# Kernel tuning notes

Measured on AMD Instinct MI355X. Metric: run time of the kernel, lower is better.

The kernel has to match this reference:

```python
import jax, jax.numpy as jnp
import numpy as np

N = 50000
E = 1600000
IN_F = 512
OUT_F = 128
NEG_SLOPE = 0.01   # nn.LeakyReLU() default
TEMPERATURE = 0.5


def setup_inputs() -> dict:
    key = jax.random.key(0)
    k1, k2, k3, k4 = jax.random.split(key, 4)
    h = jax.random.normal(k1, (N, IN_F), dtype=jnp.float32)
    # xavier_uniform with gain=1.414
    limW = 1.414 * np.sqrt(6.0 / (IN_F + OUT_F))
    W = jax.random.uniform(k2, (IN_F, OUT_F), minval=-limW, maxval=limW, dtype=jnp.float32)
    lima = 1.414 * np.sqrt(6.0 / (2 * OUT_F + 1))
    a = jax.random.uniform(k3, (2 * OUT_F, 1), minval=-lima, maxval=lima, dtype=jnp.float32)
    edge_index = jax.random.randint(k4, (2, E), 0, N, dtype=jnp.int64)
    return {"h": h, "W": W, "a": a, "edge_index": edge_index}


def reference(h, W, a, edge_index):
    # Inference: F.dropout(training=False) is identity.
    Wh = h @ W                                   # [N, F_out]
    src = edge_index[0]                          # row indices -> softmax segments
    dst = edge_index[1]
    # cat([Wh[src], Wh[dst]]) @ a == (Wh @ a1)[src] + (Wh @ a2)[dst]
    a1 = a[:OUT_F, 0]
    a2 = a[OUT_F:, 0]
    s1 = Wh @ a1                                 # [N]
    s2 = Wh @ a2                                 # [N]
    e = s1[src] + s2[dst]                        # [E]
    e = jnp.where(e >= 0, e, NEG_SLOPE * e)      # LeakyReLU
    logits = e / TEMPERATURE
    # sparse softmax over dim=1 (per source-node row segments)
    seg_max = jax.ops.segment_max(logits, src, num_segments=N)  # [N]
    ex = jnp.exp(logits - seg_max[src])          # [E]
    denom = jax.ops.segment_sum(ex, src, num_segments=N)        # [N]
    att = ex / denom[src]                        # [E]
    # sparse-dense matmul: h_prime[i] = sum_j att(i,j) * Wh[j]
    h_prime = jax.ops.segment_sum(att[:, None] * Wh[dst], src, num_segments=N)  # [N, F_out]
    return jax.nn.relu(h_prime)                  # concat=True path
```

## Files before the change

### kernel.cpp

```cpp
#include <hip/hip_runtime.h>
#include <cstdint>
#include <cstddef>

#define N_NODES 50000
#define N_EDGES 1600000
#define IN_FEAT 512
#define OUT_FEAT 128
#define NEG_SLOPE 0.01f
#define INV_TEMP 2.0f
#define PAD_DEG 128

#define BUCKETS 400
#define BNODES 125
#define BCAP 5000
#define A_BLOCKS 250
#define A_EPC (N_EDGES / A_BLOCKS)
#define A_G4 (A_EPC / 4)

typedef __attribute__((ext_vector_type(8))) short short8;
typedef __attribute__((ext_vector_type(4))) float f32x4;

#define GLOBAL_AS __attribute__((address_space(1)))
#define LDS_AS __attribute__((address_space(3)))

__device__ inline unsigned short f2bf(float x) {
    unsigned int u = __float_as_uint(x);
    unsigned int r = (u + 0x7fffu + ((u >> 16) & 1u)) >> 16;
    return (unsigned short)r;
}
__device__ inline float bf2f(unsigned short b) {
    return __uint_as_float(((unsigned int)b) << 16);
}


__global__ __launch_bounds__(256) void binA_kernel(const int* __restrict__ src,
                                                   const int* __restrict__ dst,
                                                   int* __restrict__ bucket_cursor,
                                                   int* __restrict__ binned) {
    __shared__ int cntL[BUCKETS];
    __shared__ int baseL[BUCKETS];
    int t = threadIdx.x;
    for (int i = t; i < BUCKETS; i += 256) cntL[i] = 0;
    __syncthreads();
    size_t ebase = (size_t)blockIdx.x * A_EPC;

    for (int g = t; g < A_G4; g += 256) {
        int4 s4 = *(const int4*)(src + ebase + (size_t)g * 4);
#pragma unroll
        for (int j = 0; j < 4; ++j) {
            int s = (&s4.x)[j];
            atomicAdd(&cntL[s / BNODES], 1);
        }
    }
    __syncthreads();
    for (int i = t; i < BUCKETS; i += 256) {
        int c = cntL[i];
        baseL[i] = c ? atomicAdd(&bucket_cursor[i], c) : 0;
        cntL[i] = 0;
    }
    __syncthreads();
    for (int g = t; g < A_G4; g += 256) {
        int4 s4 = *(const int4*)(src + ebase + (size_t)g * 4);
        int4 d4 = *(const int4*)(dst + ebase + (size_t)g * 4);
#pragma unroll
        for (int j = 0; j < 4; ++j) {
            int s = (&s4.x)[j];
            int b = s / BNODES;
            int sl = s - b * BNODES;
            int pos = atomicAdd(&cntL[b], 1);
            int slot = baseL[b] + pos;
            if (slot < BCAP)
                binned[(size_t)b * BCAP + slot] = (sl << 16) | (&d4.x)[j];
        }
    }
}


__global__ __launch_bounds__(256) void binB_kernel(const int* __restrict__ bucket_cursor,
                                                   const int* __restrict__ binned,
                                                   int* __restrict__ cnt,
                                                   int* __restrict__ csr) {
    __shared__ int cL[BNODES];
    int b = blockIdx.x;
    int t = threadIdx.x;
    if (t < BNODES) cL[t] = 0;
    __syncthreads();
    int m = min(bucket_cursor[b], BCAP);
    const int* bp = binned + (size_t)b * BCAP;
    int n0 = b * BNODES;
    for (int i = t; i < m; i += 256) {
        int p = bp[i];
        int sl = p >> 16;
        int d = p & 0xFFFF;
        int pos = atomicAdd(&cL[sl], 1);
        if (pos < PAD_DEG) csr[(size_t)(n0 + sl) * PAD_DEG + pos] = d;
    }
    __syncthreads();
    if (t < BNODES) cnt[n0 + t] = min(cL[t], PAD_DEG);
}

__global__ __launch_bounds__(256) void convert_w_kernel(const float* __restrict__ W,
                                                        unsigned short* __restrict__ Wt,
                                                        int* __restrict__ bucket_cursor) {
    int tid = blockIdx.x * blockDim.x + threadIdx.x;
    if (tid < BUCKETS) bucket_cursor[tid] = 0;
    if (tid >= IN_FEAT * OUT_FEAT) return;
    int n = tid >> 9;
    int k = tid & 511;
    Wt[tid] = f2bf(W[k * OUT_FEAT + n]);
}


__global__ __launch_bounds__(256) void mfma_gemm_kernel(const float* __restrict__ h,
                                                        const unsigned short* __restrict__ Wt,
                                                        const float* __restrict__ a_vec,
                                                        unsigned short* __restrict__ Whb,
                                                        float* __restrict__ s1,
                                                        float* __restrict__ s2) {
    __shared__ unsigned short lB[2][8 * 2 * 64 * 8];

    int t = threadIdx.x;
    int w = t >> 6;
    int L = t & 63;
    int m0 = blockIdx.x * 64;

    int arow = m0 + w * 16 + (L & 15);
    bool arow_ok = arow < N_NODES;
    int kq = (L >> 4) * 8;
    const float* arp = h + (size_t)arow * IN_FEAT + kq;

    f32x4 acc[8];
#pragma unroll
    for (int i = 0; i < 8; ++i) acc[i] = (f32x4){0.f, 0.f, 0.f, 0.f};

    auto stageB = [&](int buf, int k0) {
#pragma unroll
        for (int c = 0; c < 4; ++c) {
            int nb = w * 2 + (c >> 1);
            int ksub = c & 1;
            const GLOBAL_AS unsigned short* g =
                (const GLOBAL_AS unsigned short*)(Wt + (size_t)(nb * 16 + (L & 15)) * IN_FEAT +
                                                  (k0 + ksub * 32 + kq));
            LDS_AS unsigned short* lp = (LDS_AS unsigned short*)(&lB[buf][(nb * 2 + ksub) * 512]);
            __builtin_amdgcn_global_load_lds((const GLOBAL_AS void*)g, (LDS_AS void*)lp, 16, 0, 0);
        }
    };

    float4 av[2][2];
#pragma unroll
    for (int c = 0; c < 2; ++c) {
        av[c][0] = make_float4(0.f, 0.f, 0.f, 0.f);
        av[c][1] = make_float4(0.f, 0.f, 0.f, 0.f);
    }
    if (arow_ok) {
        av[0][0] = *(const float4*)(arp);
        av[0][1] = *(const float4*)(arp + 4);
        av[1][0] = *(const float4*)(arp + 32);
        av[1][1] = *(const float4*)(arp + 36);
    }
    stageB(0, 0);
    __syncthreads();

#pragma unroll
    for (int it = 0; it < 8; ++it) {
        const int buf = it & 1;

        if (it < 7) stageB(buf ^ 1, (it + 1) * 64);

        float4 avn[2][2];
#pragma unroll
        for (int c = 0; c < 2; ++c) {
            avn[c][0] = make_float4(0.f, 0.f, 0.f, 0.f);
            avn[c][1] = make_float4(0.f, 0.f, 0.f, 0.f);
        }
        if (it < 7 && arow_ok) {
            const float* p = arp + (it + 1) * 64;
            avn[0][0] = *(const float4*)(p);
            avn[0][1] = *(const float4*)(p + 4);
            avn[1][0] = *(const float4*)(p + 32);
            avn[1][1] = *(const float4*)(p + 36);
        }

        short8 af[2];
#pragma unroll
        for (int c = 0; c < 2; ++c) {
            short8 v;
            v[0] = (short)f2bf(av[c][0].x); v[1] = (short)f2bf(av[c][0].y);
            v[2] = (short)f2bf(av[c][0].z); v[3] = (short)f2bf(av[c][0].w);
            v[4] = (short)f2bf(av[c][1].x); v[5] = (short)f2bf(av[c][1].y);
            v[6] = (short)f2bf(av[c][1].z); v[7] = (short)f2bf(av[c][1].w);
            af[c] = v;
        }

#pragma unroll
        for (int ksub = 0; ksub < 2; ++ksub) {
#pragma unroll
            for (int nb = 0; nb < 8; ++nb) {
                short8 bf = *(const short8*)(&lB[buf][((nb * 2 + ksub) * 64 + L) * 8]);
                acc[nb] = __builtin_amdgcn_mfma_f32_16x16x32_bf16(af[ksub], bf, acc[nb], 0, 0, 0);
            }
        }

        __syncthreads();
#pragma unroll
        for (int c = 0; c < 2; ++c) {
            av[c][0] = avn[c][0];
            av[c][1] = avn[c][1];
        }
    }

    int col0 = L & 15;
    int rbase = m0 + w * 16 + (L >> 4) * 4;

    float a1c[8], a2c[8];
#pragma unroll
    for (int nb = 0; nb < 8; ++nb) {
        a1c[nb] = a_vec[nb * 16 + col0];
        a2c[nb] = a_vec[128 + nb * 16 + col0];
    }

#pragma unroll
    for (int r = 0; r < 4; ++r) {
        int row = rbase + r;
        bool ok = row < N_NODES;
        float p1 = 0.f, p2 = 0.f;
        if (ok) {
            unsigned short* orow = Whb + (size_t)row * OUT_FEAT;
#pragma unroll
            for (int nb = 0; nb < 8; ++nb) {
                float v = acc[nb][r];
                orow[nb * 16 + col0] = f2bf(v);
                p1 = fmaf(v, a1c[nb], p1);
                p2 = fmaf(v, a2c[nb], p2);
            }
        }
#pragma unroll
        for (int off = 8; off > 0; off >>= 1) {
            p1 += __shfl_xor(p1, off, 64);
            p2 += __shfl_xor(p2, off, 64);
        }
        if (ok && col0 == 0) {
            s1[row] = p1;
            s2[row] = p2;
        }
    }
}


__global__ __launch_bounds__(256) void node_kernel(const unsigned short* __restrict__ Whb,
                                                   const float* __restrict__ s1,
                                                   const float* __restrict__ s2,
                                                   const int* __restrict__ cnt,
                                                   const int* __restrict__ csr,
                                                   float* __restrict__ out) {
    int lane = threadIdx.x & 63;
    int w = threadIdx.x >> 6;
    int n = blockIdx.x * 4 + w;
    if (n >= N_NODES) return;
    int deg = cnt[n];
    size_t start = (size_t)n * PAD_DEG;
    int g = lane >> 4;
    int fo = lane & 15;

    float accv[8];
#pragma unroll
    for (int f = 0; f < 8; ++f) accv[f] = 0.f;
    float inv = 0.f;

    if (deg > 0) {
        float s1n = s1[n];
        int d0 = 0, d1 = 0;
        float ex0 = 0.f, ex1 = 0.f;
        if (lane < deg) {
            d0 = csr[start + lane];
            float ev = s1n + s2[d0];
            ev = ev >= 0.f ? ev : NEG_SLOPE * ev;
            ex0 = __expf(ev * INV_TEMP);
        }
        if (lane + 64 < deg) {
            d1 = csr[start + lane + 64];
            float ev = s1n + s2[d1];
            ev = ev >= 0.f ? ev : NEG_SLOPE * ev;
            ex1 = __expf(ev * INV_TEMP);
        }
        float denom = ex0 + ex1;
#pragma unroll
        for (int off = 32; off > 0; off >>= 1) denom += __shfl_xor(denom, off, 64);
        inv = 1.0f / denom;

#pragma unroll 2
        for (int jj = 0; jj < deg; jj += 4) {
            int e = jj + g;
            bool hi = jj >= 64;
            float exs = hi ? ex1 : ex0;
            int dsel = hi ? d1 : d0;
            float p = __shfl(exs, e & 63, 64);
            int dd = __shfl(dsel, e & 63, 64);
            short8 row = *(const short8*)(Whb + (size_t)dd * OUT_FEAT + fo * 8);
#pragma unroll
            for (int f = 0; f < 8; ++f)
                accv[f] = fmaf(p, bf2f((unsigned short)row[f]), accv[f]);
        }
#pragma unroll
        for (int f = 0; f < 8; ++f) {
            accv[f] += __shfl_xor(accv[f], 16, 64);
            accv[f] += __shfl_xor(accv[f], 32, 64);
        }
    }

    if (g == 0) {
        float* orow = out + (size_t)n * OUT_FEAT + fo * 8;
        float4 o0, o1;
        o0.x = fmaxf(accv[0] * inv, 0.f); o0.y = fmaxf(accv[1] * inv, 0.f);
        o0.z = fmaxf(accv[2] * inv, 0.f); o0.w = fmaxf(accv[3] * inv, 0.f);
        o1.x = fmaxf(accv[4] * inv, 0.f); o1.y = fmaxf(accv[5] * inv, 0.f);
        o1.z = fmaxf(accv[6] * inv, 0.f); o1.w = fmaxf(accv[7] * inv, 0.f);
        *(float4*)(orow) = o0;
        *(float4*)(orow + 4) = o1;
    }
}


extern "C" void kernel_launch(void* const* d_in, const int* in_sizes, int n_in,
                              void* d_out, int out_size, void* d_ws, size_t ws_size,
                              hipStream_t stream) {
    const float* h = (const float*)d_in[0];
    const float* W = (const float*)d_in[1];
    const float* a = (const float*)d_in[2];
    const int* edge = (const int*)d_in[3];
    const int* src = edge;
    const int* dst = edge + N_EDGES;
    float* out = (float*)d_out;

    char* ws = (char*)d_ws;
    size_t off = 0;
    auto alloc = [&](size_t bytes) -> void* {
        void* p = ws + off;
        off = (off + bytes + 255) & ~(size_t)255;
        return p;
    };
    unsigned short* Whb = (unsigned short*)alloc((size_t)N_NODES * OUT_FEAT * sizeof(unsigned short));
    float* s1 = (float*)alloc((size_t)N_NODES * sizeof(float));
    float* s2 = (float*)alloc((size_t)N_NODES * sizeof(float));
    int* cnt = (int*)alloc((size_t)N_NODES * sizeof(int));
    int* csr = (int*)alloc((size_t)N_NODES * PAD_DEG * sizeof(int));
    unsigned short* Wt = (unsigned short*)alloc((size_t)IN_FEAT * OUT_FEAT * sizeof(unsigned short));
    int* bucket_cursor = (int*)alloc((size_t)BUCKETS * sizeof(int));
    int* binned = (int*)alloc((size_t)BUCKETS * BCAP * sizeof(int));

    convert_w_kernel<<<(IN_FEAT * OUT_FEAT + 255) / 256, 256, 0, stream>>>(W, Wt, bucket_cursor);
    binA_kernel<<<A_BLOCKS, 256, 0, stream>>>(src, dst, bucket_cursor, binned);
    binB_kernel<<<BUCKETS, 256, 0, stream>>>(bucket_cursor, binned, cnt, csr);
    mfma_gemm_kernel<<<(N_NODES + 63) / 64, 256, 0, stream>>>(h, Wt, a, Whb, s1, s2);
    node_kernel<<<(N_NODES + 3) / 4, 256, 0, stream>>>(Whb, s1, s2, cnt, csr, out);
}
```

Baseline: 267.3 us.

## Merge independent preprocessing kernels into combined launches to cut launch count

The W conversion now runs inside the edge-binning kernel as extra blocks, and the per-bucket CSR build runs inside the GEMM kernel as leading blocks. The bucket cursor is zeroed with a memset instead of inside the conversion kernel. This cuts the number of kernel launches and the serial gaps between them, and lets unrelated work share the GPU at the same time. In exchange, each merged kernel carries branch divergence at block level, and the binB blocks take on the GEMM kernel's LDS footprint, which may reduce occupancy.

Result: no change. 262.8 us (-1.7%).

```diff
diff --git a/kernel.cpp b/kernel.cpp
--- a/kernel.cpp
+++ b/kernel.cpp
@@ -17,6 +17,9 @@
 #define A_EPC (N_EDGES / A_BLOCKS)
 #define A_G4 (A_EPC / 4)
 
+#define CONV_BLOCKS ((IN_FEAT * OUT_FEAT) / 256)
+#define GEMM_BLOCKS ((N_NODES + 63) / 64)
+
 typedef __attribute__((ext_vector_type(8))) short short8;
 typedef __attribute__((ext_vector_type(4))) float f32x4;
 
@@ -33,12 +36,25 @@
 }
 
 
-__global__ __launch_bounds__(256) void binA_kernel(const int* __restrict__ src,
-                                                   const int* __restrict__ dst,
-                                                   int* __restrict__ bucket_cursor,
-                                                   int* __restrict__ binned) {
+__global__ __launch_bounds__(256) void build_kernel(const float* __restrict__ W,
+                                                    unsigned short* __restrict__ Wt,
+                                                    const int* __restrict__ src,
+                                                    const int* __restrict__ dst,
+                                                    int* __restrict__ bucket_cursor,
+                                                    int* __restrict__ binned) {
     __shared__ int cntL[BUCKETS];
     __shared__ int baseL[BUCKETS];
+
+    if (blockIdx.x >= A_BLOCKS) {
+        int tid = (blockIdx.x - A_BLOCKS) * 256 + threadIdx.x;
+        if (tid < IN_FEAT * OUT_FEAT) {
+            int n = tid >> 9;
+            int k = tid & 511;
+            Wt[tid] = f2bf(W[k * OUT_FEAT + n]);
+        }
+        return;
+    }
+
     int t = threadIdx.x;
     for (int i = t; i < BUCKETS; i += 256) cntL[i] = 0;
     __syncthreads();
@@ -76,53 +92,44 @@
 }
 
 
-__global__ __launch_bounds__(256) void binB_kernel(const int* __restrict__ bucket_cursor,
-                                                   const int* __restrict__ binned,
-                                                   int* __restrict__ cnt,
-                                                   int* __restrict__ csr) {
-    __shared__ int cL[BNODES];
-    int b = blockIdx.x;
-    int t = threadIdx.x;
-    if (t < BNODES) cL[t] = 0;
-    __syncthreads();
-    int m = min(bucket_cursor[b], BCAP);
-    const int* bp = binned + (size_t)b * BCAP;
-    int n0 = b * BNODES;
-    for (int i = t; i < m; i += 256) {
-        int p = bp[i];
-        int sl = p >> 16;
-        int d = p & 0xFFFF;
-        int pos = atomicAdd(&cL[sl], 1);
-        if (pos < PAD_DEG) csr[(size_t)(n0 + sl) * PAD_DEG + pos] = d;
-    }
-    __syncthreads();
-    if (t < BNODES) cnt[n0 + t] = min(cL[t], PAD_DEG);
-}
-
-__global__ __launch_bounds__(256) void convert_w_kernel(const float* __restrict__ W,
-                                                        unsigned short* __restrict__ Wt,
-                                                        int* __restrict__ bucket_cursor) {
-    int tid = blockIdx.x * blockDim.x + threadIdx.x;
-    if (tid < BUCKETS) bucket_cursor[tid] = 0;
-    if (tid >= IN_FEAT * OUT_FEAT) return;
-    int n = tid >> 9;
-    int k = tid & 511;
-    Wt[tid] = f2bf(W[k * OUT_FEAT + n]);
-}
-
-
-__global__ __launch_bounds__(256) void mfma_gemm_kernel(const float* __restrict__ h,
+__global__ __launch_bounds__(256) void gemm_binB_kernel(const float* __restrict__ h,
                                                         const unsigned short* __restrict__ Wt,
                                                         const float* __restrict__ a_vec,
                                                         unsigned short* __restrict__ Whb,
                                                         float* __restrict__ s1,
-                                                        float* __restrict__ s2) {
+                                                        float* __restrict__ s2,
+                                                        const int* __restrict__ bucket_cursor,
+                                                        const int* __restrict__ binned,
+                                                        int* __restrict__ cnt,
+                                                        int* __restrict__ csr) {
     __shared__ unsigned short lB[2][8 * 2 * 64 * 8];
 
+    if (blockIdx.x < BUCKETS) {
+        int* cL = (int*)&lB[0][0];
+        int b = blockIdx.x;
+        int t = threadIdx.x;
+        if (t < BNODES) cL[t] = 0;
+        __syncthreads();
+        int m = min(bucket_cursor[b], BCAP);
+        const int* bp = binned + (size_t)b * BCAP;
+        int n0 = b * BNODES;
+        for (int i = t; i < m; i += 256) {
+            int p = bp[i];
+            int sl = p >> 16;
+            int d = p & 0xFFFF;
+            int pos = atomicAdd(&cL[sl], 1);
+            if (pos < PAD_DEG) csr[(size_t)(n0 + sl) * PAD_DEG + pos] = d;
+        }
+        __syncthreads();
+        if (t < BNODES) cnt[n0 + t] = min(cL[t], PAD_DEG);
+        return;
+    }
+
+    int bid = blockIdx.x - BUCKETS;
     int t = threadIdx.x;
     int w = t >> 6;
     int L = t & 63;
-    int m0 = blockIdx.x * 64;
+    int m0 = bid * 64;
 
     int arow = m0 + w * 16 + (L & 15);
     bool arow_ok = arow < N_NODES;
@@ -348,9 +355,9 @@
     int* bucket_cursor = (int*)alloc((size_t)BUCKETS * sizeof(int));
     int* binned = (int*)alloc((size_t)BUCKETS * BCAP * sizeof(int));
 
-    convert_w_kernel<<<(IN_FEAT * OUT_FEAT + 255) / 256, 256, 0, stream>>>(W, Wt, bucket_cursor);
-    binA_kernel<<<A_BLOCKS, 256, 0, stream>>>(src, dst, bucket_cursor, binned);
-    binB_kernel<<<BUCKETS, 256, 0, stream>>>(bucket_cursor, binned, cnt, csr);
-    mfma_gemm_kernel<<<(N_NODES + 63) / 64, 256, 0, stream>>>(h, Wt, a, Whb, s1, s2);
+    hipMemsetAsync(bucket_cursor, 0, BUCKETS * sizeof(int), stream);
+    build_kernel<<<A_BLOCKS + CONV_BLOCKS, 256, 0, stream>>>(W, Wt, src, dst, bucket_cursor, binned);
+    gemm_binB_kernel<<<BUCKETS + GEMM_BLOCKS, 256, 0, stream>>>(h, Wt, a, Whb, s1, s2,
+                                                                bucket_cursor, binned, cnt, csr);
     node_kernel<<<(N_NODES + 3) / 4, 256, 0, stream>>>(Whb, s1, s2, cnt, csr, out);
 }
```
